# Performance work log

Measured on AMD Instinct MI355X. Metric: run time of the kernel, lower is better.

## Reference

```python
import jax, jax.numpy as jnp
import numpy as np

ALPHA = 0.2
TOP_K = 32

def setup_inputs() -> dict:
    key = jax.random.key(0)
    k1, k2, k3, k4, k5 = jax.random.split(key, 5)
    B, T, N, D = 2, 12, 8192, 256
    X = jax.random.normal(k1, (B, T, N, D), dtype=jnp.float32)
    E1 = jax.random.normal(k2, (N, D), dtype=jnp.float32)
    E2 = jax.random.normal(k3, (N, D), dtype=jnp.float32)
    theta1 = jax.random.normal(k4, (D, D), dtype=jnp.float32)
    theta2 = jax.random.normal(k5, (D, D), dtype=jnp.float32)
    a = jnp.float32(1.0)
    return {"X": X, "E1": E1, "E2": E2, "theta1": theta1, "theta2": theta2, "a": a}

def reference(X, E1, E2, theta1, theta2, a):
    # X: [B, T, N, D]
    N = X.shape[2]
    X0 = X.mean(axis=1)[0]  # [N, D], mean over time, first batch element
    # Row-wise L2 normalize (F.normalize with eps=1e-12)
    norm = jnp.maximum(jnp.linalg.norm(X0, axis=1, keepdims=True), 1e-12)
    X_norm = X0 / norm
    sim = X_norm @ X_norm.T  # [N, N] cosine similarity
    sim = sim * (1.0 - jnp.eye(N, dtype=sim.dtype))  # zero diagonal
    topk_vals, topk_idx = jax.lax.top_k(sim, TOP_K)  # [N, K]
    rows = jnp.arange(N)[:, None]
    A_base = jnp.zeros_like(sim).at[rows, topk_idx].set(topk_vals)
    # Adaptive dependency matrix
    M1 = jnp.tanh(ALPHA * (E1 @ theta1))  # [N, D]
    M2 = jnp.tanh(ALPHA * (E2 @ theta2))  # [N, D]
    diff = M1 @ M2.T - M2 @ M1.T  # [N, N], antisymmetric
    adaptive = jax.nn.relu(jnp.tanh(a * diff))
    return adaptive * A_base
```

## Files before the change

kernel.cpp:

```cpp
#include <hip/hip_runtime.h>
#include <hip/hip_bf16.h>
#include <hip/hip_fp16.h>
#include <float.h>
#include <math.h>

#define NN 8192
#define DD 256
#define TT 12
#define TOPK 32
#define NQ 4
#define CAP 56
#define UCAP 64
#define TAU0 0.146875f
#define B2 2.2e-3f
#define DIFFCUT 3.0f

typedef __attribute__((ext_vector_type(8))) _Float16 f16x8;
typedef __attribute__((ext_vector_type(16))) float f32x16;
typedef __attribute__((ext_vector_type(4))) float f32x4;

__device__ __forceinline__ unsigned short f2h(float x) {
    __half h = __float2half(x);
    return *(unsigned short*)&h;
}
__device__ __forceinline__ float h2f(unsigned short v) {
    __half h = *(__half*)&v;
    return __half2float(h);
}

__global__ __launch_bounds__(256) void k_mean_norm(const float* __restrict__ X,
                                                   float* __restrict__ Xn,
                                                   unsigned short* __restrict__ Xpk) {
    const int row = blockIdx.x;
    const int d = threadIdx.x;
    const float* base = X + (size_t)row * DD + d;
    double s = 0.0;
#pragma unroll
    for (int t = 0; t < TT; ++t) s += (double)base[(size_t)t * NN * DD];
    const double mean = s / 12.0;

    double ss = mean * mean;
#pragma unroll
    for (int o = 32; o > 0; o >>= 1) ss += __shfl_down(ss, o, 64);
    __shared__ double wss[4];
    const int lane = threadIdx.x & 63, w = threadIdx.x >> 6;
    if (lane == 0) wss[w] = ss;
    __syncthreads();
    double nrm = sqrt(wss[0] + wss[1] + wss[2] + wss[3]);
    if (nrm < 1e-12) nrm = 1e-12;
    const float xv = (float)(mean / nrm);
    Xn[(size_t)row * DD + d] = xv;

    const int cb = row >> 5;
    const int ks = d >> 4;
    const int l = (row & 31) + 32 * ((d >> 3) & 1);
    const int e = d & 7;
    Xpk[(((size_t)cb * 16 + ks) * 64 + l) * 8 + e] = f2h(xv);
}

__global__ __launch_bounds__(512, 4) void k_simcand_M(
    const unsigned short* __restrict__ Xpk,
    const float* __restrict__ E1, const float* __restrict__ E2,
    const float* __restrict__ th1, const float* __restrict__ th2,
    float* __restrict__ M1, float* __restrict__ M2,
    unsigned int* __restrict__ Mpk,
    unsigned short* __restrict__ cand, float* __restrict__ candv,
    int* __restrict__ counts, float* __restrict__ out) {
    __shared__ __align__(16) unsigned char smem[32768];

    const int tid = threadIdx.x;

    if (blockIdx.x < 512) {
        int* cnt = (int*)smem;
        unsigned short* lst = (unsigned short*)(smem + 256);
        float* lstv = (float*)(smem + 256 + 64 * CAP * 2);

        const int w = tid >> 6, lane = tid & 63;
        const int mt = w >> 2, nt = w & 3;
        const int bx = blockIdx.x & 127;
        const int quarter = blockIdx.x >> 7;
        const int r0 = bx * 64;

        for (int i = tid; i < 64; i += 512) cnt[i] = 0;

        const f32x4 zz = {0.f, 0.f, 0.f, 0.f};
        f32x4* zp = (f32x4*)out + ((size_t)blockIdx.x * 32768) + tid;

        f16x8 afr[16];
        {
            const size_t abase = (((size_t)(bx * 2 + mt)) * 16) * 512 + lane * 8;
#pragma unroll
            for (int ks = 0; ks < 16; ++ks)
                afr[ks] = *(const f16x8*)(Xpk + abase + ks * 512);
        }
        __syncthreads();

        const int rowL = mt * 32 + ((lane >> 5) << 2);
        const int colL = lane & 31;

        for (int c = 0; c < 16; ++c) {
            const int cbB = quarter * 64 + c * 4 + nt;
            const int gcol = cbB * 32 + colL;
            const size_t bbase = ((size_t)cbB * 16) * 512 + lane * 8;

            f32x16 acc;
#pragma unroll
            for (int q = 0; q < 16; ++q) acc[q] = 0.f;
#pragma unroll
            for (int ks = 0; ks < 16; ++ks) {
                f16x8 b = *(const f16x8*)(Xpk + bbase + ks * 512);
                acc = __builtin_amdgcn_mfma_f32_32x32x16_f16(afr[ks], b, acc, 0, 0, 0);
            }

#pragma unroll
            for (int q = 0; q < 4; ++q)
                __builtin_nontemporal_store(zz, zp + (c * 4 + q) * 512);

#pragma unroll
            for (int reg = 0; reg < 16; ++reg) {
                const float v = acc[reg];
                if (v > TAU0) {
                    const int rl = rowL + (reg & 3) + ((reg >> 2) << 3);
                    if (r0 + rl != gcol) {
                        const int idx = atomicAdd(&cnt[rl], 1);
                        if (idx < CAP) {
                            lst[rl * CAP + idx] = (unsigned short)gcol;
                            lstv[rl * CAP + idx] = v;
                        }
                    }
                }
            }
        }
        __syncthreads();
        for (int i = tid; i < 64; i += 512) {
            int n = cnt[i];
            counts[(r0 + i) * NQ + quarter] = n > CAP ? CAP : n;
        }
        for (int i = tid; i < 64 * CAP; i += 512) {
            const int rl = i / CAP, k = i % CAP;
            int n = cnt[rl];
            if (n > CAP) n = CAP;
            if (k < n) {
                const size_t o = ((size_t)(r0 + rl) * NQ + quarter) * CAP + k;
                cand[o] = lst[rl * CAP + k];
                candv[o] = lstv[rl * CAP + k];
            }
        }
    } else {
        float* e1 = (float*)smem;
        float* e2 = (float*)(smem + 16384);
        const int r0 = (blockIdx.x - 512) * 16;
        for (int i = tid; i < 16 * DD; i += 512) {
            e1[i] = E1[(size_t)r0 * DD + i];
            e2[i] = E2[(size_t)r0 * DD + i];
        }
        __syncthreads();
        const int half = tid >> 8;
        const int j = tid & 255;
        const int rb = half * 8;
        float a1[8], a2[8];
#pragma unroll
        for (int r = 0; r < 8; ++r) { a1[r] = 0.f; a2[r] = 0.f; }
        for (int k = 0; k < DD; ++k) {
            const float t1 = th1[k * DD + j];
            const float t2 = th2[k * DD + j];
#pragma unroll
            for (int r = 0; r < 8; ++r) {
                a1[r] += e1[(rb + r) * DD + k] * t1;
                a2[r] += e2[(rb + r) * DD + k] * t2;
            }
        }
#pragma unroll
        for (int r = 0; r < 8; ++r) {
            const float m1v = tanhf(0.2f * a1[r]);
            const float m2v = tanhf(0.2f * a2[r]);
            M1[(size_t)(r0 + rb + r) * DD + j] = m1v;
            M2[(size_t)(r0 + rb + r) * DD + j] = m2v;
            Mpk[(size_t)(r0 + rb + r) * DD + j] =
                ((unsigned)f2h(m2v) << 16) | (unsigned)f2h(m1v);
        }
    }
}

__global__ __launch_bounds__(256) void k_refine(
    const float* __restrict__ Xn, const unsigned short* __restrict__ cand,
    const float* __restrict__ candv, const int* __restrict__ counts,
    const float* __restrict__ M1, const float* __restrict__ M2,
    const unsigned int* __restrict__ Mpk, const float* __restrict__ a_ptr,
    float* __restrict__ out) {
    __shared__ float xi[DD], m1i[DD], m2i[DD];
    __shared__ unsigned short cidx[NQ * CAP];
    __shared__ float cs[NQ * CAP];
    __shared__ int carr[NQ], offs[NQ + 1];
    __shared__ unsigned short uidx[UCAP];
    __shared__ float ue[UCAP];
    __shared__ int nUs, ms;
    __shared__ float wv[TOPK];
    __shared__ int wj[TOPK];

    const int i = blockIdx.x, t = threadIdx.x;

    xi[t]  = Xn[(size_t)i * DD + t];
    m1i[t] = M1[(size_t)i * DD + t];
    m2i[t] = M2[(size_t)i * DD + t];
    if (t < NQ) {
        int n = counts[i * NQ + t];
        carr[t] = n < 0 ? 0 : (n > CAP ? CAP : n);
    }
    if (t < TOPK) { wv[t] = 0.f; wj[t] = i; }
    if (t == 0) { nUs = 0; ms = 0; }
    __syncthreads();
    if (t == 0) {
        int s = 0;
#pragma unroll
        for (int q = 0; q < NQ; ++q) { offs[q] = s; s += carr[q]; }
        offs[NQ] = s;
    }
    __syncthreads();
    const int nc = offs[NQ];
#pragma unroll
    for (int q = 0; q < NQ; ++q)
        if (t < carr[q]) {
            const size_t o = ((size_t)i * NQ + q) * CAP + t;
            cidx[offs[q] + t] = cand[o];
            cs[offs[q] + t] = candv[o];
        }
    __syncthreads();

    if (t < nc) {
        const float vc = cs[t];
        int possAbove = 0, certAbove = 0;
        for (int k = 0; k < nc; ++k) {
            const float vk = cs[k];
            possAbove += (vk >= vc - B2);
            certAbove += (vk > vc + B2);
        }
        possAbove -= 1;
        if (possAbove <= TOPK - 1) {
            const int slot = atomicAdd(&ms, 1);
            wv[slot] = vc;
            wj[slot] = cidx[t];
        } else if (certAbove < TOPK) {
            const int p = atomicAdd(&nUs, 1);
            if (p < UCAP) uidx[p] = cidx[t];
        }
    }
    __syncthreads();
    const int m = ms;
    int nU = nUs;
    if (nU > UCAP) nU = UCAP;

    if (nU > 0) {
        const int dl = t & 15, cg = t >> 4;
        for (int base = 0; base < nU; base += 16) {
            const int c = base + cg;
            float p = 0.f;
            if (c < nU) {
                const int j = uidx[c];
                const f32x4* xj4 = (const f32x4*)(Xn + (size_t)j * DD) + dl * 4;
                const f32x4* xi4 = (const f32x4*)xi + dl * 4;
#pragma unroll
                for (int q = 0; q < 4; ++q) {
                    const f32x4 A = xi4[q], B = xj4[q];
                    p += A.x * B.x;
                    p += A.y * B.y;
                    p += A.z * B.z;
                    p += A.w * B.w;
                }
            }
#pragma unroll
            for (int o = 1; o < 16; o <<= 1) p += __shfl_xor(p, o, 64);
            if (c < nU && dl == 0) ue[c] = p;
        }
        __syncthreads();
        if (t < nU && m < TOPK) {
            const float vc = ue[t];
            const int jc = uidx[t];
            int r = 0;
            for (int k = 0; k < nU; ++k) {
                const float vk = ue[k];
                r += (vk > vc) || (vk == vc && uidx[k] < jc);
            }
            if (r < TOPK - m) {
                wv[m + r] = vc;
                wj[m + r] = jc;
            }
        }
        __syncthreads();
    }

    const float a = *a_ptr;
    const int g = t >> 3, lg = t & 7;
    const int j = wj[g];
    const float v = wv[g];

    float p1 = 0.f;
    {
        const uint4* mp = (const uint4*)(Mpk + (size_t)j * DD) + lg * 8;
#pragma unroll
        for (int q = 0; q < 8; ++q) {
            const uint4 u = mp[q];
            const int d = lg * 32 + q * 4;
            p1 += m1i[d + 0] * h2f((unsigned short)(u.x >> 16)) -
                  m2i[d + 0] * h2f((unsigned short)(u.x & 0xffff));
            p1 += m1i[d + 1] * h2f((unsigned short)(u.y >> 16)) -
                  m2i[d + 1] * h2f((unsigned short)(u.y & 0xffff));
            p1 += m1i[d + 2] * h2f((unsigned short)(u.z >> 16)) -
                  m2i[d + 2] * h2f((unsigned short)(u.z & 0xffff));
            p1 += m1i[d + 3] * h2f((unsigned short)(u.w >> 16)) -
                  m2i[d + 3] * h2f((unsigned short)(u.w & 0xffff));
        }
    }
#pragma unroll
    for (int o = 4; o > 0; o >>= 1) p1 += __shfl_xor(p1, o, 64);

    float diff = p1;
    if (fabsf(diff) < DIFFCUT) {
        const f32x4* m1j4 = (const f32x4*)(M1 + (size_t)j * DD) + lg * 8;
        const f32x4* m2j4 = (const f32x4*)(M2 + (size_t)j * DD) + lg * 8;
        float p = 0.f;
        const int dbase = lg * 32;
#pragma unroll
        for (int q = 0; q < 8; ++q) {
            const f32x4 b1 = m1j4[q], b2 = m2j4[q];
            const int d = dbase + q * 4;
            p += m1i[d + 0] * b2.x - m2i[d + 0] * b1.x;
            p += m1i[d + 1] * b2.y - m2i[d + 1] * b1.y;
            p += m1i[d + 2] * b2.z - m2i[d + 2] * b1.z;
            p += m1i[d + 3] * b2.w - m2i[d + 3] * b1.w;
        }
#pragma unroll
        for (int o = 4; o > 0; o >>= 1) p += __shfl_xor(p, o, 64);
        diff = p;
    }
    if (lg == 0 && j != i) {
        float ad = tanhf(a * diff);
        ad = ad > 0.f ? ad : 0.f;
        out[(size_t)i * NN + j] = ad * v;
    }
}

extern "C" void kernel_launch(void* const* d_in, const int* in_sizes, int n_in,
                              void* d_out, int out_size, void* d_ws, size_t ws_size,
                              hipStream_t stream) {
    const float* X   = (const float*)d_in[0];
    const float* E1  = (const float*)d_in[1];
    const float* E2  = (const float*)d_in[2];
    const float* th1 = (const float*)d_in[3];
    const float* th2 = (const float*)d_in[4];
    const float* a   = (const float*)d_in[5];
    float* out = (float*)d_out;

    float* ws = (float*)d_ws;
    float* Xn = ws;
    float* M1 = Xn + (size_t)NN * DD;
    float* M2 = M1 + (size_t)NN * DD;
    unsigned short* Xpk = (unsigned short*)(M2 + (size_t)NN * DD);
    unsigned int* Mpk = (unsigned int*)(Xpk + (size_t)NN * DD);
    unsigned short* cand = (unsigned short*)(Mpk + (size_t)NN * DD);
    float* candv = (float*)(cand + (size_t)NN * NQ * CAP);
    int* counts = (int*)(candv + (size_t)NN * NQ * CAP);

    k_mean_norm<<<NN, 256, 0, stream>>>(X, Xn, Xpk);
    k_simcand_M<<<512 + 512, 512, 0, stream>>>(Xpk, E1, E2, th1, th2,
                                               M1, M2, Mpk,
                                               cand, candv, counts, out);
    k_refine<<<NN, 256, 0, stream>>>(Xn, cand, candv, counts, M1, M2, Mpk, a, out);
}
```

Baseline: 241.3 us.

## Split similarity blocks finer, use global atomics, interleave GEMM blocks, vectorize loads

Each similarity block now covers half as many column blocks, which doubles the number of similarity blocks. These blocks are interleaved with the M-projection blocks in a 2:1 pattern across a 1536-block grid. Candidates go straight to global memory through global atomics on per-row, per-quarter counters, which k_mean_norm now zeroes; this removes the shared-memory staging, its barriers and the copy-out loop. Output zeroing is rewritten so stores are row-contiguous, and the E1/E2 staging and the theta GEMM inner loop use vector loads. The risks are global atomic contention and the counts no longer being clamped to CAP, so k_refine may see values above CAP.

```diff
diff --git a/kernel.cpp b/kernel.cpp
--- a/kernel.cpp
+++ b/kernel.cpp
@@ -30,9 +30,11 @@
 
 __global__ __launch_bounds__(256) void k_mean_norm(const float* __restrict__ X,
                                                    float* __restrict__ Xn,
-                                                   unsigned short* __restrict__ Xpk) {
+                                                   unsigned short* __restrict__ Xpk,
+                                                   int* __restrict__ counts) {
     const int row = blockIdx.x;
     const int d = threadIdx.x;
+    if (d < NQ) counts[row * NQ + d] = 0;
     const float* base = X + (size_t)row * DD + d;
     double s = 0.0;
 #pragma unroll
@@ -69,22 +71,17 @@
     __shared__ __align__(16) unsigned char smem[32768];
 
     const int tid = threadIdx.x;
-
-    if (blockIdx.x < 512) {
-        int* cnt = (int*)smem;
-        unsigned short* lst = (unsigned short*)(smem + 256);
-        float* lstv = (float*)(smem + 256 + 64 * CAP * 2);
+    const int m3 = blockIdx.x % 3;
+
+    if (m3 != 2) {
+        const int simIdx = (blockIdx.x / 3) * 2 + m3;
+        const int bx = simIdx & 127;
+        const int g = simIdx >> 7;
+        const int quarter = g >> 1;
+        const int r0 = bx * 64;
 
         const int w = tid >> 6, lane = tid & 63;
         const int mt = w >> 2, nt = w & 3;
-        const int bx = blockIdx.x & 127;
-        const int quarter = blockIdx.x >> 7;
-        const int r0 = bx * 64;
-
-        for (int i = tid; i < 64; i += 512) cnt[i] = 0;
-
-        const f32x4 zz = {0.f, 0.f, 0.f, 0.f};
-        f32x4* zp = (f32x4*)out + ((size_t)blockIdx.x * 32768) + tid;
 
         f16x8 afr[16];
         {
@@ -93,13 +90,16 @@
             for (int ks = 0; ks < 16; ++ks)
                 afr[ks] = *(const f16x8*)(Xpk + abase + ks * 512);
         }
-        __syncthreads();
 
         const int rowL = mt * 32 + ((lane >> 5) << 2);
         const int colL = lane & 31;
 
-        for (int c = 0; c < 16; ++c) {
-            const int cbB = quarter * 64 + c * 4 + nt;
+        const f32x4 zz = {0.f, 0.f, 0.f, 0.f};
+        const int zr = tid >> 5, zc = tid & 31;
+        f32x4* zbase = (f32x4*)out + ((size_t)(r0 + zr)) * 2048 + g * 256 + zc;
+
+        for (int c = 0; c < 8; ++c) {
+            const int cbB = g * 32 + c * 4 + nt;
             const int gcol = cbB * 32 + colL;
             const size_t bbase = ((size_t)cbB * 16) * 512 + lane * 8;
 
@@ -114,7 +114,7 @@
 
 #pragma unroll
             for (int q = 0; q < 4; ++q)
-                __builtin_nontemporal_store(zz, zp + (c * 4 + q) * 512);
+                __builtin_nontemporal_store(zz, zbase + (size_t)q * 16 * 2048 + c * 32);
 
 #pragma unroll
             for (int reg = 0; reg < 16; ++reg) {
@@ -122,37 +122,29 @@
                 if (v > TAU0) {
                     const int rl = rowL + (reg & 3) + ((reg >> 2) << 3);
                     if (r0 + rl != gcol) {
-                        const int idx = atomicAdd(&cnt[rl], 1);
-                        if (idx < CAP) {
-                            lst[rl * CAP + idx] = (unsigned short)gcol;
-                            lstv[rl * CAP + idx] = v;
+                        const int p = atomicAdd(&counts[(r0 + rl) * NQ + quarter], 1);
+                        if (p < CAP) {
+                            const size_t o = ((size_t)(r0 + rl) * NQ + quarter) * CAP + p;
+                            cand[o] = (unsigned short)gcol;
+                            candv[o] = v;
                         }
                     }
                 }
             }
         }
-        __syncthreads();
-        for (int i = tid; i < 64; i += 512) {
-            int n = cnt[i];
-            counts[(r0 + i) * NQ + quarter] = n > CAP ? CAP : n;
-        }
-        for (int i = tid; i < 64 * CAP; i += 512) {
-            const int rl = i / CAP, k = i % CAP;
-            int n = cnt[rl];
-            if (n > CAP) n = CAP;
-            if (k < n) {
-                const size_t o = ((size_t)(r0 + rl) * NQ + quarter) * CAP + k;
-                cand[o] = lst[rl * CAP + k];
-                candv[o] = lstv[rl * CAP + k];
-            }
-        }
     } else {
         float* e1 = (float*)smem;
         float* e2 = (float*)(smem + 16384);
-        const int r0 = (blockIdx.x - 512) * 16;
-        for (int i = tid; i < 16 * DD; i += 512) {
-            e1[i] = E1[(size_t)r0 * DD + i];
-            e2[i] = E2[(size_t)r0 * DD + i];
+        const int r0 = (blockIdx.x / 3) * 16;
+        {
+            const f32x4* E14 = (const f32x4*)(E1 + (size_t)r0 * DD);
+            const f32x4* E24 = (const f32x4*)(E2 + (size_t)r0 * DD);
+            f32x4* e14 = (f32x4*)e1;
+            f32x4* e24 = (f32x4*)e2;
+            for (int i = tid; i < 1024; i += 512) {
+                e14[i] = E14[i];
+                e24[i] = E24[i];
+            }
         }
         __syncthreads();
         const int half = tid >> 8;
@@ -161,13 +153,25 @@
         float a1[8], a2[8];
 #pragma unroll
         for (int r = 0; r < 8; ++r) { a1[r] = 0.f; a2[r] = 0.f; }
-        for (int k = 0; k < DD; ++k) {
-            const float t1 = th1[k * DD + j];
-            const float t2 = th2[k * DD + j];
+        for (int k = 0; k < DD; k += 4) {
+            float t1[4], t2[4];
+#pragma unroll
+            for (int kk = 0; kk < 4; ++kk) {
+                t1[kk] = th1[(size_t)(k + kk) * DD + j];
+                t2[kk] = th2[(size_t)(k + kk) * DD + j];
+            }
 #pragma unroll
             for (int r = 0; r < 8; ++r) {
-                a1[r] += e1[(rb + r) * DD + k] * t1;
-                a2[r] += e2[(rb + r) * DD + k] * t2;
+                const f32x4 ev1 = *(const f32x4*)&e1[(rb + r) * DD + k];
+                const f32x4 ev2 = *(const f32x4*)&e2[(rb + r) * DD + k];
+                a1[r] += ev1.x * t1[0];
+                a1[r] += ev1.y * t1[1];
+                a1[r] += ev1.z * t1[2];
+                a1[r] += ev1.w * t1[3];
+                a2[r] += ev2.x * t2[0];
+                a2[r] += ev2.y * t2[1];
+                a2[r] += ev2.z * t2[2];
+                a2[r] += ev2.w * t2[3];
             }
         }
 #pragma unroll
@@ -361,9 +365,9 @@
     float* candv = (float*)(cand + (size_t)NN * NQ * CAP);
     int* counts = (int*)(candv + (size_t)NN * NQ * CAP);
 
-    k_mean_norm<<<NN, 256, 0, stream>>>(X, Xn, Xpk);
-    k_simcand_M<<<512 + 512, 512, 0, stream>>>(Xpk, E1, E2, th1, th2,
-                                               M1, M2, Mpk,
-                                               cand, candv, counts, out);
+    k_mean_norm<<<NN, 256, 0, stream>>>(X, Xn, Xpk, counts);
+    k_simcand_M<<<1536, 512, 0, stream>>>(Xpk, E1, E2, th1, th2,
+                                          M1, M2, Mpk,
+                                          cand, candv, counts, out);
     k_refine<<<NN, 256, 0, stream>>>(Xn, cand, candv, counts, M1, M2, Mpk, a, out);
 }
```

Result: slower. 354.9 us (+47.1%).
